# Optimization experiments

Hardware: AMD Instinct MI355X
Metric: run time of the kernel (lower is better)

The kernel has to match this reference:

```python
import jax, jax.numpy as jnp
import numpy as np

B, L, HEAD_IN, DIM = 16, 512, 4, 64
HEAD_OUT = 4


def setup_inputs() -> dict:
    key = jax.random.key(0)
    k1, k2 = jax.random.split(key)
    inp = jax.random.normal(k1, (B, L, HEAD_IN, DIM), dtype=jnp.float32)
    # one (dim x dim) 'general' attention weight per (head_out, head_in) pair
    W = jax.random.normal(k2, (HEAD_OUT, HEAD_IN, DIM, DIM), dtype=jnp.float32) / np.sqrt(DIM)
    return {"inp": inp, "W": W}


def reference(inp, W):
    # inp: [b, l, j(head_in), d]; W: [o(head_out), j, d, e]
    b, l, j, d = inp.shape
    scale = 1.0 / jnp.sqrt(jnp.asarray(d, inp.dtype))
    # q_ij = x_j @ W_ij  -> [o, j, b, l, e]
    q = jnp.einsum('bljd,ojde->ojble', inp, W)
    # scores_ij = q_ij @ x_j^T / sqrt(d) -> [o, j, b, l, m]
    scores = jnp.einsum('ojble,bmje->ojblm', q, inp) * scale
    attn = jax.nn.softmax(scores, axis=-1)          # [o, j, b, l, m]
    ctx = jnp.einsum('ojblm,bmjd->ojbld', attn, inp)  # [o, j, b, l, d]
    out = jnp.mean(ctx, axis=1)                      # mean over head_in -> [o, b, l, d]
    out = jnp.transpose(out, (1, 2, 0, 3))           # [b, l, head_out, d]
    return out, attn
```

## Files before the change

### kernel.cpp

```cpp
#include <hip/hip_runtime.h>
#include <stdint.h>


typedef __bf16 bf16x8 __attribute__((ext_vector_type(8)));
typedef float  f32x4  __attribute__((ext_vector_type(4)));
typedef unsigned int u32;
typedef u32 u32x4 __attribute__((ext_vector_type(4)));

#define XRM_OFF 0
#define XCM_OFF 65536
#define WT_OFF  131072
#define QB_OFF  140288
#define LDS_BYTES 158720

static __device__ __forceinline__ u32 f2bf(float f) {
    u32 u = __builtin_bit_cast(u32, f);
    u += 0x7fffu + ((u >> 16) & 1u);
    return u >> 16;
}
static __device__ __forceinline__ float bflo2f(u32 p) { return __builtin_bit_cast(float, p << 16); }
static __device__ __forceinline__ float bfhi2f(u32 p) { return __builtin_bit_cast(float, p & 0xffff0000u); }

__global__ __launch_bounds__(512, 2) void convattn_kernel(
    const float* __restrict__ inp,
    const float* __restrict__ Wg,
    float* __restrict__ out)
{
    extern __shared__ __align__(16) char smem[];
    const int tid  = threadIdx.x;
    const int wave = tid >> 6;
    const int lane = tid & 63;
    const int g    = lane >> 4;
    const int ln   = lane & 15;
    const int rl   = lane >> 2;
    const int rq   = lane & 3;

    const int bid = blockIdx.x;
    const int b  = bid & 15;
    const int o  = (bid >> 4) & 3;
    const int lt = bid >> 6;
    const int l0 = lt * 128 + wave * 16;

    float* attn_out = out + (size_t)2097152;
    char* qb = smem + QB_OFF + wave * 2304;

    f32x4 acc_c[4];
    #pragma unroll
    for (int i = 0; i < 4; ++i) { f32x4 z = {0.f,0.f,0.f,0.f}; acc_c[i] = z; }

    #pragma unroll 1
    for (int j = 0; j < 4; ++j) {
        __syncthreads();

        {
            const int q = tid & 15, p = tid >> 4;
            const int e0 = q << 2;
            #pragma unroll
            for (int it = 0; it < 8; ++it) {
                const int m0 = it * 64 + p * 2;
                const float* src = inp + (((size_t)b * 512 + m0) * 4 + j) * 64 + e0;
                const float4 va = *(const float4*)src;
                const float4 vb = *(const float4*)(src + 256);
                const u32 pa0 = f2bf(va.x), pa1 = f2bf(va.y), pa2 = f2bf(va.z), pa3 = f2bf(va.w);
                const u32 pb0 = f2bf(vb.x), pb1 = f2bf(vb.y), pb2 = f2bf(vb.z), pb3 = f2bf(vb.w);
                {
                    uint2 w0; w0.x = pa0 | (pa1 << 16); w0.y = pa2 | (pa3 << 16);
                    *(uint2*)(smem + XRM_OFF + m0 * 128 + (((q >> 1) ^ (m0 & 7)) * 16) + ((q & 1) * 8)) = w0;
                    uint2 w1; w1.x = pb0 | (pb1 << 16); w1.y = pb2 | (pb3 << 16);
                    *(uint2*)(smem + XRM_OFF + (m0 + 1) * 128 + (((q >> 1) ^ ((m0 + 1) & 7)) * 16) + ((q & 1) * 8)) = w1;
                }
                const u32 pc[4] = { pa0 | (pb0 << 16), pa1 | (pb1 << 16),
                                    pa2 | (pb2 << 16), pa3 | (pb3 << 16) };
                #pragma unroll
                for (int c = 0; c < 4; ++c) {
                    const int d = e0 + c;
                    *(u32*)(smem + XCM_OFF + d * 1024 + (((m0 >> 3) ^ ((d >> 2) & 7)) * 16) + (m0 & 7) * 2) = pc[c];
                }
            }
            #pragma unroll
            for (int it = 0; it < 2; ++it) {
                const int d = it * 32 + p;
                const float4 wv = *(const float4*)(Wg + (((size_t)o * 4 + j) * 64 + d) * 64 + e0);
                *(unsigned short*)(smem + WT_OFF + (e0 + 0) * 144 + d * 2) = (unsigned short)f2bf(wv.x);
                *(unsigned short*)(smem + WT_OFF + (e0 + 1) * 144 + d * 2) = (unsigned short)f2bf(wv.y);
                *(unsigned short*)(smem + WT_OFF + (e0 + 2) * 144 + d * 2) = (unsigned short)f2bf(wv.z);
                *(unsigned short*)(smem + WT_OFF + (e0 + 3) * 144 + d * 2) = (unsigned short)f2bf(wv.w);
            }
        }
        __syncthreads();

        {
            const int lq = l0 + ln;
            const bf16x8 aq0 = *(const bf16x8*)(smem + XRM_OFF + lq * 128 + (((0 + g) ^ (lq & 7)) * 16));
            const bf16x8 aq1 = *(const bf16x8*)(smem + XRM_OFF + lq * 128 + (((4 + g) ^ (lq & 7)) * 16));
            #pragma unroll
            for (int et = 0; et < 4; ++et) {
                const int e = et * 16 + ln;
                const bf16x8 bw0 = *(const bf16x8*)(smem + WT_OFF + e * 144 + g * 16);
                const bf16x8 bw1 = *(const bf16x8*)(smem + WT_OFF + e * 144 + 64 + g * 16);
                f32x4 t = {0.f,0.f,0.f,0.f};
                t = __builtin_amdgcn_mfma_f32_16x16x32_bf16(aq0, bw0, t, 0, 0, 0);
                t = __builtin_amdgcn_mfma_f32_16x16x32_bf16(aq1, bw1, t, 0, 0, 0);
                #pragma unroll
                for (int r = 0; r < 4; ++r)
                    *(unsigned short*)(qb + (g * 4 + r) * 144 + e * 2) = (unsigned short)f2bf(t[r]);
            }
        }
        const bf16x8 bq0 = *(const bf16x8*)(qb + ln * 144 + g * 16);
        const bf16x8 bq1 = *(const bf16x8*)(qb + ln * 144 + 64 + g * 16);

        float mx = -3.402823466e+38f;
        #pragma unroll
        for (int mt = 0; mt < 32; ++mt) {
            const int m = mt * 16 + ln;
            const bf16x8 ax0 = *(const bf16x8*)(smem + XRM_OFF + m * 128 + (((0 + g) ^ (m & 7)) * 16));
            const bf16x8 ax1 = *(const bf16x8*)(smem + XRM_OFF + m * 128 + (((4 + g) ^ (m & 7)) * 16));
            f32x4 t = {0.f,0.f,0.f,0.f};
            t = __builtin_amdgcn_mfma_f32_16x16x32_bf16(ax0, bq0, t, 0, 0, 0);
            t = __builtin_amdgcn_mfma_f32_16x16x32_bf16(ax1, bq1, t, 0, 0, 0);
            mx = fmaxf(mx, fmaxf(fmaxf(t[0], t[1]), fmaxf(t[2], t[3])));
        }
        mx = fmaxf(mx, __shfl_xor(mx, 16, 64));
        mx = fmaxf(mx, __shfl_xor(mx, 32, 64));

        float sum = 0.f;
        u32 sLo[32], sHi[32];
        #pragma unroll
        for (int mt = 0; mt < 32; ++mt) {
            const int m = mt * 16 + ln;
            const bf16x8 ax0 = *(const bf16x8*)(smem + XRM_OFF + m * 128 + (((0 + g) ^ (m & 7)) * 16));
            const bf16x8 ax1 = *(const bf16x8*)(smem + XRM_OFF + m * 128 + (((4 + g) ^ (m & 7)) * 16));
            f32x4 t = {0.f,0.f,0.f,0.f};
            t = __builtin_amdgcn_mfma_f32_16x16x32_bf16(ax0, bq0, t, 0, 0, 0);
            t = __builtin_amdgcn_mfma_f32_16x16x32_bf16(ax1, bq1, t, 0, 0, 0);
            const float e0v = __expf((t[0] - mx) * 0.125f);
            const float e1v = __expf((t[1] - mx) * 0.125f);
            const float e2v = __expf((t[2] - mx) * 0.125f);
            const float e3v = __expf((t[3] - mx) * 0.125f);
            sum += (e0v + e1v) + (e2v + e3v);
            sLo[mt] = f2bf(e0v) | (f2bf(e1v) << 16);
            sHi[mt] = f2bf(e2v) | (f2bf(e3v) << 16);
        }
        sum += __shfl_xor(sum, 16, 64);
        sum += __shfl_xor(sum, 32, 64);
        const float inv = 1.0f / sum;

        const size_t abase = ((size_t)((o * 4 + j) * 16 + b)) * 262144 + (size_t)l0 * 512;
        const int srcLo = ((g & 1) << 5) + ln;
        const int srcHi = srcLo + 16;
        #pragma unroll
        for (int ch = 0; ch < 16; ++ch) {
            u32 pLo[2], pHi[2];
            #pragma unroll
            for (int s = 0; s < 2; ++s) {
                const int mt = ch * 2 + s;
                const float a0v = bflo2f(sLo[mt]) * inv;
                const float a1v = bfhi2f(sLo[mt]) * inv;
                const float a2v = bflo2f(sHi[mt]) * inv;
                const float a3v = bfhi2f(sHi[mt]) * inv;
                *(float*)(qb + ln * 80 + (g * 4 + 0) * 4) = a0v;
                *(float*)(qb + ln * 80 + (g * 4 + 1) * 4) = a1v;
                *(float*)(qb + ln * 80 + (g * 4 + 2) * 4) = a2v;
                *(float*)(qb + ln * 80 + (g * 4 + 3) * 4) = a3v;
                const f32x4 rv = *(const f32x4*)(qb + rl * 80 + rq * 16);
                __builtin_nontemporal_store(rv,
                    (f32x4*)(attn_out + abase + (size_t)rl * 512 + mt * 16 + rq * 4));
                pLo[s] = f2bf(a0v) | (f2bf(a1v) << 16);
                pHi[s] = f2bf(a2v) | (f2bf(a3v) << 16);
            }
            const u32 a0s = (u32)__shfl((int)pLo[0], srcLo, 64);
            const u32 a1s = (u32)__shfl((int)pHi[0], srcLo, 64);
            const u32 a2s = (u32)__shfl((int)pLo[0], srcHi, 64);
            const u32 a3s = (u32)__shfl((int)pHi[0], srcHi, 64);
            const u32 b0s = (u32)__shfl((int)pLo[1], srcLo, 64);
            const u32 b1s = (u32)__shfl((int)pHi[1], srcLo, 64);
            const u32 b2s = (u32)__shfl((int)pLo[1], srcHi, 64);
            const u32 b3s = (u32)__shfl((int)pHi[1], srcHi, 64);
            const bool hi = (g >= 2);
            const u32 dw0 = hi ? b0s : a0s;
            const u32 dw1 = hi ? b1s : a1s;
            const u32 dw2 = hi ? b2s : a2s;
            const u32 dw3 = hi ? b3s : a3s;
            const bf16x8 bfrag = __builtin_bit_cast(bf16x8, (u32x4){dw0, dw1, dw2, dw3});
            #pragma unroll
            for (int dt = 0; dt < 4; ++dt) {
                const int d = dt * 16 + ln;
                const bf16x8 ax = *(const bf16x8*)(smem + XCM_OFF + d * 1024 +
                                   (((ch * 4 + g) ^ ((d >> 2) & 7)) * 16));
                acc_c[dt] = __builtin_amdgcn_mfma_f32_16x16x32_bf16(ax, bfrag, acc_c[dt], 0, 0, 0);
            }
        }
    }

    #pragma unroll
    for (int dt = 0; dt < 4; ++dt) {
        #pragma unroll
        for (int r = 0; r < 4; ++r)
            *(float*)(qb + ln * 80 + (g * 4 + r) * 4) = acc_c[dt][r] * 0.25f;
        const f32x4 rv = *(const f32x4*)(qb + rl * 80 + rq * 16);
        *(f32x4*)(out + (((size_t)b * 512 + (l0 + rl)) * 4 + o) * 64 + dt * 16 + rq * 4) = rv;
    }
}

extern "C" void kernel_launch(void* const* d_in, const int* in_sizes, int n_in,
                              void* d_out, int out_size, void* d_ws, size_t ws_size,
                              hipStream_t stream) {
    const float* inp = (const float*)d_in[0];
    const float* Wg  = (const float*)d_in[1];
    float* out = (float*)d_out;
    (void)hipFuncSetAttribute((const void*)convattn_kernel,
                              hipFuncAttributeMaxDynamicSharedMemorySize, LDS_BYTES);
    convattn_kernel<<<dim3(256), dim3(512), LDS_BYTES, stream>>>(inp, Wg, out);
}
```

Before: 354.8 us.

## Shrink LDS footprint, halve block size, drop softmax max pass

Blocks go from 512 to 256 threads and the grid doubles. Row-major and column-major copies of x now share one LDS buffer: the column-major copy is reloaded from global after the score pass, so LDS per block drops to about 76KB and more blocks can sit on each CU. The separate max-reduction pass over the scores is removed and exp is applied without subtracting the max, which saves one full QK^T MFMA sweep but risks overflow if scores are large. Padded Q/W staging layouts are also replaced with XOR-swizzled ones.

Result: slower. 409.2 us (+15.3%).

```diff
diff --git a/kernel.cpp b/kernel.cpp
--- a/kernel.cpp
+++ b/kernel.cpp
@@ -7,11 +7,11 @@
 typedef unsigned int u32;
 typedef u32 u32x4 __attribute__((ext_vector_type(4)));
 
-#define XRM_OFF 0
-#define XCM_OFF 65536
-#define WT_OFF  131072
-#define QB_OFF  140288
-#define LDS_BYTES 158720
+#define XB_OFF  0
+#define WT_OFF  65536
+#define QB_OFF  73728
+#define P3B_OFF 65536
+#define LDS_BYTES 77824
 
 static __device__ __forceinline__ u32 f2bf(float f) {
     u32 u = __builtin_bit_cast(u32, f);
@@ -21,7 +21,7 @@
 static __device__ __forceinline__ float bflo2f(u32 p) { return __builtin_bit_cast(float, p << 16); }
 static __device__ __forceinline__ float bfhi2f(u32 p) { return __builtin_bit_cast(float, p & 0xffff0000u); }
 
-__global__ __launch_bounds__(512, 2) void convattn_kernel(
+__global__ __launch_bounds__(256, 2) void convattn_kernel(
     const float* __restrict__ inp,
     const float* __restrict__ Wg,
     float* __restrict__ out)
@@ -39,10 +39,14 @@
     const int b  = bid & 15;
     const int o  = (bid >> 4) & 3;
     const int lt = bid >> 6;
-    const int l0 = lt * 128 + wave * 16;
+    const int l0 = lt * 64 + wave * 16;
 
     float* attn_out = out + (size_t)2097152;
-    char* qb = smem + QB_OFF + wave * 2304;
+    char* qb  = smem + QB_OFF  + wave * 1024;
+    char* p3b = smem + P3B_OFF + wave * 1280;
+
+    const int sq = tid & 15;
+    const int sp = tid >> 4;
 
     f32x4 acc_c[4];
     #pragma unroll
@@ -53,90 +57,76 @@
         __syncthreads();
 
         {
-            const int q = tid & 15, p = tid >> 4;
-            const int e0 = q << 2;
-            #pragma unroll
-            for (int it = 0; it < 8; ++it) {
-                const int m0 = it * 64 + p * 2;
+            const int e0 = sq << 2;
+            #pragma unroll
+            for (int it = 0; it < 16; ++it) {
+                const int m0 = it * 32 + sp * 2;
                 const float* src = inp + (((size_t)b * 512 + m0) * 4 + j) * 64 + e0;
                 const float4 va = *(const float4*)src;
                 const float4 vb = *(const float4*)(src + 256);
-                const u32 pa0 = f2bf(va.x), pa1 = f2bf(va.y), pa2 = f2bf(va.z), pa3 = f2bf(va.w);
-                const u32 pb0 = f2bf(vb.x), pb1 = f2bf(vb.y), pb2 = f2bf(vb.z), pb3 = f2bf(vb.w);
-                {
-                    uint2 w0; w0.x = pa0 | (pa1 << 16); w0.y = pa2 | (pa3 << 16);
-                    *(uint2*)(smem + XRM_OFF + m0 * 128 + (((q >> 1) ^ (m0 & 7)) * 16) + ((q & 1) * 8)) = w0;
-                    uint2 w1; w1.x = pb0 | (pb1 << 16); w1.y = pb2 | (pb3 << 16);
-                    *(uint2*)(smem + XRM_OFF + (m0 + 1) * 128 + (((q >> 1) ^ ((m0 + 1) & 7)) * 16) + ((q & 1) * 8)) = w1;
-                }
-                const u32 pc[4] = { pa0 | (pb0 << 16), pa1 | (pb1 << 16),
-                                    pa2 | (pb2 << 16), pa3 | (pb3 << 16) };
-                #pragma unroll
-                for (int c = 0; c < 4; ++c) {
-                    const int d = e0 + c;
-                    *(u32*)(smem + XCM_OFF + d * 1024 + (((m0 >> 3) ^ ((d >> 2) & 7)) * 16) + (m0 & 7) * 2) = pc[c];
-                }
-            }
-            #pragma unroll
-            for (int it = 0; it < 2; ++it) {
-                const int d = it * 32 + p;
-                const float4 wv = *(const float4*)(Wg + (((size_t)o * 4 + j) * 64 + d) * 64 + e0);
-                *(unsigned short*)(smem + WT_OFF + (e0 + 0) * 144 + d * 2) = (unsigned short)f2bf(wv.x);
-                *(unsigned short*)(smem + WT_OFF + (e0 + 1) * 144 + d * 2) = (unsigned short)f2bf(wv.y);
-                *(unsigned short*)(smem + WT_OFF + (e0 + 2) * 144 + d * 2) = (unsigned short)f2bf(wv.z);
-                *(unsigned short*)(smem + WT_OFF + (e0 + 3) * 144 + d * 2) = (unsigned short)f2bf(wv.w);
-            }
-        }
-        __syncthreads();
-
+                uint2 w0; w0.x = f2bf(va.x) | (f2bf(va.y) << 16); w0.y = f2bf(va.z) | (f2bf(va.w) << 16);
+                *(uint2*)(smem + XB_OFF + m0 * 128 + (((sq >> 1) ^ (m0 & 7)) * 16) + ((sq & 1) * 8)) = w0;
+                uint2 w1; w1.x = f2bf(vb.x) | (f2bf(vb.y) << 16); w1.y = f2bf(vb.z) | (f2bf(vb.w) << 16);
+                *(uint2*)(smem + XB_OFF + (m0 + 1) * 128 + (((sq >> 1) ^ ((m0 + 1) & 7)) * 16) + ((sq & 1) * 8)) = w1;
+            }
+            const int wd = tid >> 2;
+            const int we = (tid & 3) << 4;
+            const float* wsrc = Wg + (((size_t)o * 4 + j) * 64 + wd) * 64 + we;
+            #pragma unroll
+            for (int c = 0; c < 4; ++c) {
+                const float4 wv = *(const float4*)(wsrc + c * 4);
+                const int e = we + c * 4;
+                const u32 q0 = f2bf(wv.x), q1 = f2bf(wv.y), q2 = f2bf(wv.z), q3 = f2bf(wv.w);
+                *(unsigned short*)(smem + WT_OFF + (e + 0) * 128 + (((wd >> 3) ^ ((e + 0) & 7)) * 16) + ((wd & 7) * 2)) = (unsigned short)q0;
+                *(unsigned short*)(smem + WT_OFF + (e + 1) * 128 + (((wd >> 3) ^ ((e + 1) & 7)) * 16) + ((wd & 7) * 2)) = (unsigned short)q1;
+                *(unsigned short*)(smem + WT_OFF + (e + 2) * 128 + (((wd >> 3) ^ ((e + 2) & 7)) * 16) + ((wd & 7) * 2)) = (unsigned short)q2;
+                *(unsigned short*)(smem + WT_OFF + (e + 3) * 128 + (((wd >> 3) ^ ((e + 3) & 7)) * 16) + ((wd & 7) * 2)) = (unsigned short)q3;
+            }
+        }
+        __syncthreads();
+
+        bf16x8 bq0, bq1;
         {
             const int lq = l0 + ln;
-            const bf16x8 aq0 = *(const bf16x8*)(smem + XRM_OFF + lq * 128 + (((0 + g) ^ (lq & 7)) * 16));
-            const bf16x8 aq1 = *(const bf16x8*)(smem + XRM_OFF + lq * 128 + (((4 + g) ^ (lq & 7)) * 16));
-            #pragma unroll
-            for (int et = 0; et < 4; ++et) {
-                const int e = et * 16 + ln;
-                const bf16x8 bw0 = *(const bf16x8*)(smem + WT_OFF + e * 144 + g * 16);
-                const bf16x8 bw1 = *(const bf16x8*)(smem + WT_OFF + e * 144 + 64 + g * 16);
-                f32x4 t = {0.f,0.f,0.f,0.f};
-                t = __builtin_amdgcn_mfma_f32_16x16x32_bf16(aq0, bw0, t, 0, 0, 0);
-                t = __builtin_amdgcn_mfma_f32_16x16x32_bf16(aq1, bw1, t, 0, 0, 0);
+            const bf16x8 aq0 = *(const bf16x8*)(smem + XB_OFF + lq * 128 + ((g ^ (lq & 7)) * 16));
+            const bf16x8 aq1 = *(const bf16x8*)(smem + XB_OFF + lq * 128 + (((4 + g) ^ (lq & 7)) * 16));
+            #pragma unroll
+            for (int h = 0; h < 2; ++h) {
                 #pragma unroll
-                for (int r = 0; r < 4; ++r)
-                    *(unsigned short*)(qb + (g * 4 + r) * 144 + e * 2) = (unsigned short)f2bf(t[r]);
-            }
-        }
-        const bf16x8 bq0 = *(const bf16x8*)(qb + ln * 144 + g * 16);
-        const bf16x8 bq1 = *(const bf16x8*)(qb + ln * 144 + 64 + g * 16);
-
-        float mx = -3.402823466e+38f;
-        #pragma unroll
-        for (int mt = 0; mt < 32; ++mt) {
-            const int m = mt * 16 + ln;
-            const bf16x8 ax0 = *(const bf16x8*)(smem + XRM_OFF + m * 128 + (((0 + g) ^ (m & 7)) * 16));
-            const bf16x8 ax1 = *(const bf16x8*)(smem + XRM_OFF + m * 128 + (((4 + g) ^ (m & 7)) * 16));
-            f32x4 t = {0.f,0.f,0.f,0.f};
-            t = __builtin_amdgcn_mfma_f32_16x16x32_bf16(ax0, bq0, t, 0, 0, 0);
-            t = __builtin_amdgcn_mfma_f32_16x16x32_bf16(ax1, bq1, t, 0, 0, 0);
-            mx = fmaxf(mx, fmaxf(fmaxf(t[0], t[1]), fmaxf(t[2], t[3])));
-        }
-        mx = fmaxf(mx, __shfl_xor(mx, 16, 64));
-        mx = fmaxf(mx, __shfl_xor(mx, 32, 64));
+                for (int et = 0; et < 2; ++et) {
+                    const int e = h * 32 + et * 16 + ln;
+                    const bf16x8 bw0 = *(const bf16x8*)(smem + WT_OFF + e * 128 + ((g ^ (e & 7)) * 16));
+                    const bf16x8 bw1 = *(const bf16x8*)(smem + WT_OFF + e * 128 + (((4 + g) ^ (e & 7)) * 16));
+                    f32x4 t = {0.f,0.f,0.f,0.f};
+                    t = __builtin_amdgcn_mfma_f32_16x16x32_bf16(aq0, bw0, t, 0, 0, 0);
+                    t = __builtin_amdgcn_mfma_f32_16x16x32_bf16(aq1, bw1, t, 0, 0, 0);
+                    const int cell = et * 2 + (ln >> 3);
+                    #pragma unroll
+                    for (int r = 0; r < 4; ++r) {
+                        const int lr = g * 4 + r;
+                        *(unsigned short*)(qb + lr * 64 + ((cell ^ (lr & 3)) * 16) + ((ln & 7) * 2)) = (unsigned short)f2bf(t[r]);
+                    }
+                }
+                const bf16x8 bq = *(const bf16x8*)(qb + ln * 64 + ((g ^ (ln & 3)) * 16));
+                if (h == 0) bq0 = bq; else bq1 = bq;
+                __builtin_amdgcn_sched_barrier(0);
+            }
+        }
 
         float sum = 0.f;
         u32 sLo[32], sHi[32];
         #pragma unroll
         for (int mt = 0; mt < 32; ++mt) {
             const int m = mt * 16 + ln;
-            const bf16x8 ax0 = *(const bf16x8*)(smem + XRM_OFF + m * 128 + (((0 + g) ^ (m & 7)) * 16));
-            const bf16x8 ax1 = *(const bf16x8*)(smem + XRM_OFF + m * 128 + (((4 + g) ^ (m & 7)) * 16));
+            const bf16x8 ax0 = *(const bf16x8*)(smem + XB_OFF + m * 128 + ((g ^ (m & 7)) * 16));
+            const bf16x8 ax1 = *(const bf16x8*)(smem + XB_OFF + m * 128 + (((4 + g) ^ (m & 7)) * 16));
             f32x4 t = {0.f,0.f,0.f,0.f};
             t = __builtin_amdgcn_mfma_f32_16x16x32_bf16(ax0, bq0, t, 0, 0, 0);
             t = __builtin_amdgcn_mfma_f32_16x16x32_bf16(ax1, bq1, t, 0, 0, 0);
-            const float e0v = __expf((t[0] - mx) * 0.125f);
-            const float e1v = __expf((t[1] - mx) * 0.125f);
-            const float e2v = __expf((t[2] - mx) * 0.125f);
-            const float e3v = __expf((t[3] - mx) * 0.125f);
+            const float e0v = __expf(t[0] * 0.125f);
+            const float e1v = __expf(t[1] * 0.125f);
+            const float e2v = __expf(t[2] * 0.125f);
+            const float e3v = __expf(t[3] * 0.125f);
             sum += (e0v + e1v) + (e2v + e3v);
             sLo[mt] = f2bf(e0v) | (f2bf(e1v) << 16);
             sHi[mt] = f2bf(e2v) | (f2bf(e3v) << 16);
@@ -144,6 +134,30 @@
         sum += __shfl_xor(sum, 16, 64);
         sum += __shfl_xor(sum, 32, 64);
         const float inv = 1.0f / sum;
+
+        __syncthreads();
+
+        {
+            const int e0 = sq << 2;
+            #pragma unroll
+            for (int it = 0; it < 16; ++it) {
+                const int m0 = it * 32 + sp * 2;
+                const float* src = inp + (((size_t)b * 512 + m0) * 4 + j) * 64 + e0;
+                const float4 va = *(const float4*)src;
+                const float4 vb = *(const float4*)(src + 256);
+                const u32 p0 = f2bf(va.x) | (f2bf(vb.x) << 16);
+                const u32 p1 = f2bf(va.y) | (f2bf(vb.y) << 16);
+                const u32 p2 = f2bf(va.z) | (f2bf(vb.z) << 16);
+                const u32 p3v = f2bf(va.w) | (f2bf(vb.w) << 16);
+                const u32 pc[4] = {p0, p1, p2, p3v};
+                #pragma unroll
+                for (int c = 0; c < 4; ++c) {
+                    const int d = e0 + c;
+                    *(u32*)(smem + XB_OFF + d * 1024 + (((m0 >> 3) ^ ((d >> 2) & 7)) * 16) + ((m0 & 7) * 2)) = pc[c];
+                }
+            }
+        }
+        __syncthreads();
 
         const size_t abase = ((size_t)((o * 4 + j) * 16 + b)) * 262144 + (size_t)l0 * 512;
         const int srcLo = ((g & 1) << 5) + ln;
@@ -158,11 +172,11 @@
                 const float a1v = bfhi2f(sLo[mt]) * inv;
                 const float a2v = bflo2f(sHi[mt]) * inv;
                 const float a3v = bfhi2f(sHi[mt]) * inv;
-                *(float*)(qb + ln * 80 + (g * 4 + 0) * 4) = a0v;
-                *(float*)(qb + ln * 80 + (g * 4 + 1) * 4) = a1v;
-                *(float*)(qb + ln * 80 + (g * 4 + 2) * 4) = a2v;
-                *(float*)(qb + ln * 80 + (g * 4 + 3) * 4) = a3v;
-                const f32x4 rv = *(const f32x4*)(qb + rl * 80 + rq * 16);
+                *(float*)(p3b + ln * 80 + (g * 4 + 0) * 4) = a0v;
+                *(float*)(p3b + ln * 80 + (g * 4 + 1) * 4) = a1v;
+                *(float*)(p3b + ln * 80 + (g * 4 + 2) * 4) = a2v;
+                *(float*)(p3b + ln * 80 + (g * 4 + 3) * 4) = a3v;
+                const f32x4 rv = *(const f32x4*)(p3b + rl * 80 + rq * 16);
                 __builtin_nontemporal_store(rv,
                     (f32x4*)(attn_out + abase + (size_t)rl * 512 + mt * 16 + rq * 4));
                 pLo[s] = f2bf(a0v) | (f2bf(a1v) << 16);
@@ -185,7 +199,7 @@
             #pragma unroll
             for (int dt = 0; dt < 4; ++dt) {
                 const int d = dt * 16 + ln;
-                const bf16x8 ax = *(const bf16x8*)(smem + XCM_OFF + d * 1024 +
+                const bf16x8 ax = *(const bf16x8*)(smem + XB_OFF + d * 1024 +
                                    (((ch * 4 + g) ^ ((d >> 2) & 7)) * 16));
                 acc_c[dt] = __builtin_amdgcn_mfma_f32_16x16x32_bf16(ax, bfrag, acc_c[dt], 0, 0, 0);
             }
@@ -196,8 +210,8 @@
     for (int dt = 0; dt < 4; ++dt) {
         #pragma unroll
         for (int r = 0; r < 4; ++r)
-            *(float*)(qb + ln * 80 + (g * 4 + r) * 4) = acc_c[dt][r] * 0.25f;
-        const f32x4 rv = *(const f32x4*)(qb + rl * 80 + rq * 16);
+            *(float*)(p3b + ln * 80 + (g * 4 + r) * 4) = acc_c[dt][r] * 0.25f;
+        const f32x4 rv = *(const f32x4*)(p3b + rl * 80 + rq * 16);
         *(f32x4*)(out + (((size_t)b * 512 + (l0 + rl)) * 4 + o) * 64 + dt * 16 + rq * 4) = rv;
     }
 }
@@ -210,5 +224,5 @@
     float* out = (float*)d_out;
     (void)hipFuncSetAttribute((const void*)convattn_kernel,
                               hipFuncAttributeMaxDynamicSharedMemorySize, LDS_BYTES);
-    convattn_kernel<<<dim3(256), dim3(512), LDS_BYTES, stream>>>(inp, Wg, out);
+    convattn_kernel<<<dim3(512), dim3(256), LDS_BYTES, stream>>>(inp, Wg, out);
 }
```
